# Kernel optimization log

Measured on AMD Instinct MI355X. Metric: run time of the kernel, lower is better.

## Reference

```python
import jax, jax.numpy as jnp
import numpy as np

B, C, H, W = 1, 12, 256, 256
T = 8          # time_steps
F = 64         # recurrent/conv filters
SIGMA = 1.0


def _to_c(x):
    return jax.lax.complex(x[..., 0], x[..., 1])


def _to_r(x):
    return jnp.stack([jnp.real(x), jnp.imag(x)], axis=-1)


def _fft2c(x):  # orthogonal centered 2D FFT over last two dims (complex input)
    x = jnp.fft.ifftshift(x, axes=(-2, -1))
    x = jnp.fft.fft2(x, axes=(-2, -1), norm='ortho')
    return jnp.fft.fftshift(x, axes=(-2, -1))


def _ifft2c(x):
    x = jnp.fft.ifftshift(x, axes=(-2, -1))
    x = jnp.fft.ifft2(x, axes=(-2, -1), norm='ortho')
    return jnp.fft.fftshift(x, axes=(-2, -1))


def _conv(x, w, b=None, dilation=1):
    k = w.shape[-1]
    pad = dilation * (k - 1) // 2  # 'same' padding as ConvNonlinear
    y = jax.lax.conv_general_dilated(x, w, (1, 1), [(pad, pad), (pad, pad)],
                                     rhs_dilation=(dilation, dilation),
                                     dimension_numbers=('NCHW', 'OIHW', 'NCHW'))
    if b is not None:
        y = y + b[None, :, None, None]
    return y


def _gru(x, h, ih_w, ih_b, hh_w, hh_b):  # ConvGRUCell
    i_r, i_z, i_n = jnp.split(_conv(x, ih_w, ih_b), 3, axis=1)
    h_r, h_z, h_n = jnp.split(_conv(h, hh_w, hh_b), 3, axis=1)
    r = jax.nn.sigmoid(i_r + h_r)
    z = jax.nn.sigmoid(i_z + h_z)
    n = jnp.tanh(i_n + r * h_n)
    return (1.0 - z) * n + z * h


def setup_inputs():
    key = jax.random.key(0)
    ks = jax.random.split(key, 16)
    rn = lambda k, s, sc=1.0: jax.random.normal(k, s, jnp.float32) * sc
    return {
        'pred': rn(ks[0], (B, C, H, W, 2)),
        'masked_kspace': rn(ks[1], (B, C, H, W, 2)),
        'sense': rn(ks[2], (B, C, H, W, 2), 0.1),
        'mask': jax.random.randint(ks[3], (B, 1, H, W, 1), 0, 2).astype(bool),
        'conv1_w': rn(ks[4], (F, 4, 5, 5), 0.05),
        'conv1_b': jnp.zeros((F,), jnp.float32),
        'gru1_ih_w': rn(ks[5], (3 * F, F, 1, 1), 0.05),
        'gru1_ih_b': jnp.zeros((3 * F,), jnp.float32),
        'gru1_hh_w': rn(ks[6], (3 * F, F, 1, 1), 0.05),
        'gru1_hh_b': jnp.zeros((3 * F,), jnp.float32),
        'conv2_w': rn(ks[7], (F, F, 3, 3), 0.05),
        'conv2_b': jnp.zeros((F,), jnp.float32),
        'gru2_ih_w': rn(ks[8], (3 * F, F, 1, 1), 0.05),
        'gru2_ih_b': jnp.zeros((3 * F,), jnp.float32),
        'gru2_hh_w': rn(ks[9], (3 * F, F, 1, 1), 0.05),
        'gru2_hh_b': jnp.zeros((3 * F,), jnp.float32),
        'final_w': rn(ks[10], (2, F, 3, 3), 0.05),
        'dc_weight': jnp.ones((1,), jnp.float32),
    }


def reference(pred, masked_kspace, sense, mask, conv1_w, conv1_b, gru1_ih_w, gru1_ih_b,
              gru1_hh_w, gru1_hh_b, conv2_w, conv2_b, gru2_ih_w, gru2_ih_b, gru2_hh_w,
              gru2_hh_b, final_w, dc_weight):
    ksp_c = _to_c(masked_kspace)   # [B,C,H,W] complex
    sense_c = _to_c(sense)
    mask_f = mask[..., 0].astype(jnp.float32)  # [B,1,H,W]
    # eta init (eta=None path): coil-combined ifft of pred
    eta0 = jnp.sum(_ifft2c(_to_c(pred)) * jnp.conj(sense_c), axis=1)  # [B,H,W]
    h1_0 = jnp.zeros((B, F, H, W), jnp.float32)
    h2_0 = jnp.zeros((B, F, H, W), jnp.float32)
    inv_s2 = 1.0 / (SIGMA * SIGMA)

    def step(carry, _):
        eta, h1, h2 = carry
        # log_likelihood_gradient: SENSE-expand, fft, masked residual, ifft, coil-combine
        resid = _ifft2c(mask_f * (_fft2c(eta[:, None] * sense_c) - ksp_c))  # [B,C,H,W]
        grad = jnp.sum(resid * jnp.conj(sense_c), axis=1)                   # [B,H,W]
        g = jnp.stack([eta.real, eta.imag, grad.real, grad.imag], axis=1) * inv_s2  # [B,4,H,W]
        h1 = _gru(jax.nn.relu(_conv(g, conv1_w, conv1_b, 1)), h1,
                  gru1_ih_w, gru1_ih_b, gru1_hh_w, gru1_hh_b)
        h2 = _gru(jax.nn.relu(_conv(h1, conv2_w, conv2_b, 2)), h2,
                  gru2_ih_w, gru2_ih_b, gru2_hh_w, gru2_hh_b)
        d = _conv(h2, final_w, None, 1)  # [B,2,H,W], no bias, no nonlinearity
        eta = eta + jax.lax.complex(d[:, 0], d[:, 1])
        return (eta, h1, h2), eta

    _, etas = jax.lax.scan(step, (eta0, h1_0, h2_0), None, length=T)  # [T,B,H,W]
    # data-consistency output per time step
    soft_dc = jnp.where(mask, pred - masked_kspace, 0.0) * dc_weight[0]  # [B,C,H,W,2]
    dc_c = _to_c(soft_dc)
    out = ksp_c[None] - dc_c[None] - _fft2c(etas[:, :, None] * sense_c[None])  # [T,B,C,H,W]
    return _to_r(out)  # [T,B,C,H,W,2]
```

## Files before the change

kernel.cpp:

```cpp
#include <hip/hip_runtime.h>

#define HW 65536
#define NC 12
#define NF 64
#define NT 8
#define P2 260

typedef float2 c32;
typedef __attribute__((ext_vector_type(8))) short bf16x8;
typedef __attribute__((ext_vector_type(4))) float f32x4;

__device__ __forceinline__ float ssign(int p) {
    return ((p ^ (p >> 8)) & 1) ? -1.0f : 1.0f;
}

__device__ __forceinline__ short f2bf(float f) {
    union { float f; unsigned u; } v; v.f = f;
    unsigned r = (v.u + 0x7FFFu + ((v.u >> 16) & 1u)) >> 16;
    return (short)r;
}

__device__ __forceinline__ float bf2f(unsigned short u) {
    union { unsigned u; float f; } v; v.u = (unsigned)u << 16;
    return v.f;
}

__device__ __forceinline__ void wave_sync() {
    asm volatile("s_waitcnt lgkmcnt(0)" ::: "memory");
}

__device__ __forceinline__ void fft256_wave(c32* X, const c32* tw, int j, float conjf) {
    #pragma unroll
    for (int s = 1; s <= 8; ++s) {
        const int half = 1 << (s - 1);
        #pragma unroll
        for (int b = 0; b < 2; ++b) {
            int idx = j + (b << 6);
            int grp = idx >> (s - 1);
            int pos = idx & (half - 1);
            int i0 = (grp << s) + pos;
            int i1 = i0 + half;
            c32 w = tw[pos << (8 - s)];
            float wy = conjf * w.y;
            c32 a = X[i0], cc = X[i1];
            c32 t = make_float2(w.x * cc.x - wy * cc.y, w.x * cc.y + wy * cc.x);
            X[i0] = make_float2(a.x + t.x, a.y + t.y);
            X[i1] = make_float2(a.x - t.x, a.y - t.y);
        }
        wave_sync();
    }
}

__device__ __forceinline__ void build_tw(c32* tw, int tid) {
    if (tid < 128) {
        float a = -3.14159265358979323846f * (float)tid * (1.0f / 128.0f);
        float sv, cv;
        sincosf(a, &sv, &cv);
        tw[tid] = make_float2(cv, sv);
    }
}

__global__ __launch_bounds__(256) void fft_rows_pre(c32* __restrict__ buf,
        const c32* __restrict__ pred) {
    __shared__ c32 lds[4][256];
    __shared__ c32 tw[128];
    int tid = threadIdx.x;
    build_tw(tw, tid);
    int wid = tid >> 6, j = tid & 63;
    int r = blockIdx.x * 4 + wid;
    int coil = r >> 8, y = r & 255;
    c32* rp = buf + (size_t)r * 256;
    c32* X = lds[wid];
    #pragma unroll
    for (int e = 0; e < 4; ++e) {
        int n = (e << 6) + j;
        float s = ((n + y) & 1) ? -1.0f : 1.0f;
        c32 pv = pred[(size_t)coil * HW + y * 256 + n];
        X[__brev((unsigned)n) >> 24] = make_float2(s * pv.x, s * pv.y);
    }
    __syncthreads();
    fft256_wave(X, tw, j, -1.0f);
    #pragma unroll
    for (int e = 0; e < 4; ++e) {
        int n = (e << 6) + j;
        rp[n] = X[n];
    }
}

__global__ __launch_bounds__(256) void fft_rows_exp(c32* __restrict__ buf,
        const c32* __restrict__ eta, const c32* __restrict__ sense) {
    __shared__ c32 lds[4][256];
    __shared__ c32 tw[128];
    int tid = threadIdx.x;
    build_tw(tw, tid);
    int wid = tid >> 6, j = tid & 63;
    int r = blockIdx.x * 4 + wid;
    int coil = r >> 8, y = r & 255;
    c32* rp = buf + (size_t)r * 256;
    c32* X = lds[wid];
    #pragma unroll
    for (int e = 0; e < 4; ++e) {
        int n = (e << 6) + j;
        float s = ((n + y) & 1) ? -1.0f : 1.0f;
        c32 ev = eta[y * 256 + n];
        c32 sn = sense[(size_t)coil * HW + y * 256 + n];
        X[__brev((unsigned)n) >> 24] =
            make_float2(s * (ev.x * sn.x - ev.y * sn.y),
                        s * (ev.x * sn.y + ev.y * sn.x));
    }
    __syncthreads();
    fft256_wave(X, tw, j, 1.0f);
    #pragma unroll
    for (int e = 0; e < 4; ++e) {
        int n = (e << 6) + j;
        rp[n] = X[n];
    }
}

__global__ __launch_bounds__(256) void fft_rows_grad(const c32* __restrict__ Fk,
        const c32* __restrict__ sense, const c32* __restrict__ eta,
        short* __restrict__ gTp) {
    __shared__ c32 lds[12][256];
    __shared__ c32 tw[128];
    int tid = threadIdx.x;
    build_tw(tw, tid);
    int wid = tid >> 6, j = tid & 63;
    int y = blockIdx.x;
    #pragma unroll
    for (int cc = 0; cc < 3; ++cc) {
        int c = wid * 3 + cc;
        const c32* rp = Fk + (size_t)c * HW + y * 256;
        #pragma unroll
        for (int e = 0; e < 4; ++e) {
            int n = (e << 6) + j;
            lds[c][__brev((unsigned)n) >> 24] = rp[n];
        }
    }
    __syncthreads();
    #pragma unroll
    for (int cc = 0; cc < 3; ++cc)
        fft256_wave(&lds[wid * 3 + cc][0], tw, j, -1.0f);
    __syncthreads();
    int x = tid;
    int p = y * 256 + x;
    float ax = 0.f, ay = 0.f;
    #pragma unroll
    for (int c = 0; c < NC; ++c) {
        c32 t = lds[c][x];
        c32 s = sense[(size_t)c * HW + p];
        ax += t.x * s.x + t.y * s.y;
        ay += t.y * s.x - t.x * s.y;
    }
    float sc = (((x + y) & 1) ? -1.0f : 1.0f) * (1.0f / 256.0f);
    c32 e = eta[p];
    ushort4 o;
    o.x = (unsigned short)f2bf(e.x);
    o.y = (unsigned short)f2bf(e.y);
    o.z = (unsigned short)f2bf(ax * sc);
    o.w = (unsigned short)f2bf(ay * sc);
    ((ushort4*)gTp)[(y + 2) * P2 + x + 2] = o;
}

__global__ __launch_bounds__(256) void fft_cols(c32* __restrict__ buf, float conjf) {
    __shared__ c32 lds[4][257];
    __shared__ c32 tw[128];
    int tid = threadIdx.x;
    build_tw(tw, tid);
    c32* ip = buf + (size_t)blockIdx.y * HW;
    int x0 = blockIdx.x * 4;
    int cl = tid & 3, yb = tid >> 2;
    #pragma unroll
    for (int e = 0; e < 4; ++e) {
        int y = yb + (e << 6);
        lds[cl][__brev((unsigned)y) >> 24] = ip[y * 256 + x0 + cl];
    }
    __syncthreads();
    int col = tid >> 6, j = tid & 63;
    fft256_wave(&lds[col][0], tw, j, conjf);
    __syncthreads();
    #pragma unroll
    for (int e = 0; e < 4; ++e) {
        int y = yb + (e << 6);
        ip[y * 256 + x0 + cl] = lds[cl][y];
    }
}

__global__ __launch_bounds__(256) void fft_cols_fused(c32* __restrict__ buf,
        const c32* __restrict__ base, const c32* __restrict__ ksp,
        const int* __restrict__ mask, c32* __restrict__ outp, int write_out) {
    __shared__ c32 lds[4][257];
    __shared__ c32 tw[128];
    int tid = threadIdx.x;
    build_tw(tw, tid);
    int coil = blockIdx.y;
    c32* ip = buf + (size_t)coil * HW;
    int x0 = blockIdx.x * 4;
    int cl = tid & 3, yb = tid >> 2;
    #pragma unroll
    for (int e = 0; e < 4; ++e) {
        int y = yb + (e << 6);
        lds[cl][__brev((unsigned)y) >> 24] = ip[y * 256 + x0 + cl];
    }
    __syncthreads();
    int col = tid >> 6, j = tid & 63;
    fft256_wave(&lds[col][0], tw, j, 1.0f);
    __syncthreads();

    int x = x0 + cl;
    c32 G[4];
    #pragma unroll
    for (int e = 0; e < 4; ++e) {
        int y = yb + (e << 6);
        G[e] = lds[cl][y];
    }
    __syncthreads();
    #pragma unroll
    for (int e = 0; e < 4; ++e) {
        int y = yb + (e << 6);
        int p = y * 256 + x;
        size_t i = (size_t)coil * HW + p;
        float s = ((p ^ (p >> 8)) & 1) ? -1.0f : 1.0f;
        if (write_out) {
            c32 bv = base[i];
            float sc = s * (1.0f / 256.0f);
            outp[i] = make_float2(bv.x - sc * G[e].x, bv.y - sc * G[e].y);
        }
        c32 rv = make_float2(0.f, 0.f);
        if (mask[p]) {
            c32 k = ksp[i];
            rv = make_float2(G[e].x * (1.0f / 256.0f) - s * k.x,
                             G[e].y * (1.0f / 256.0f) - s * k.y);
        }
        lds[cl][__brev((unsigned)y) >> 24] = rv;
    }
    __syncthreads();
    fft256_wave(&lds[col][0], tw, j, -1.0f);
    __syncthreads();
    #pragma unroll
    for (int e = 0; e < 4; ++e) {
        int y = yb + (e << 6);
        ip[y * 256 + x0 + cl] = lds[cl][y];
    }
}

__global__ __launch_bounds__(256) void k_combine_eta0(const c32* __restrict__ tmp,
        const c32* __restrict__ sense, c32* __restrict__ eta) {
    int p = blockIdx.x * 256 + threadIdx.x;
    float ax = 0.f, ay = 0.f;
    for (int c = 0; c < NC; ++c) {
        c32 t = tmp[c * HW + p], s = sense[c * HW + p];
        ax += t.x * s.x + t.y * s.y;
        ay += t.y * s.x - t.x * s.y;
    }
    float sc = ssign(p) * (1.0f / 256.0f);
    eta[p] = make_float2(ax * sc, ay * sc);
}

__global__ __launch_bounds__(256) void k_base(const c32* __restrict__ ksp,
        const c32* __restrict__ pred, const int* __restrict__ mask,
        const float* __restrict__ dcw, c32* __restrict__ base) {
    int i = blockIdx.x * 256 + threadIdx.x;
    int p = i & (HW - 1);
    c32 k = ksp[i];
    c32 o = k;
    if (mask[p]) {
        float w = dcw[0];
        c32 pr = pred[i];
        o.x -= (pr.x - k.x) * w;
        o.y -= (pr.y - k.y) * w;
    }
    base[i] = o;
}

__global__ __launch_bounds__(256) void k_zero_border(short* __restrict__ gTp,
        short* __restrict__ h1a, short* __restrict__ h1b,
        short* __restrict__ h2a, short* __restrict__ h2b) {
    int i = blockIdx.x * 256 + threadIdx.x;
    if (i >= 2064) return;
    int y, x;
    if (i < 1040) {
        int r = i / 260;
        y = (r < 2) ? r : 256 + r;
        x = i % 260;
    } else {
        int j = i - 1040;
        y = 2 + (j >> 2);
        int cix = j & 3;
        x = (cix < 2) ? cix : 256 + cix;
    }
    size_t px = (size_t)y * P2 + x;
    ((ushort4*)gTp)[px] = make_ushort4(0, 0, 0, 0);
    uint4 z = make_uint4(0, 0, 0, 0);
    uint4* p1 = (uint4*)(h1a + (px << 6));
    uint4* p2 = (uint4*)(h1b + (px << 6));
    uint4* p3 = (uint4*)(h2a + (px << 6));
    uint4* p4 = (uint4*)(h2b + (px << 6));
    #pragma unroll
    for (int e = 0; e < 8; ++e) { p1[e] = z; p2[e] = z; p3[e] = z; p4[e] = z; }
}

__global__ __launch_bounds__(256) void k_prep_c1(const float* __restrict__ w,
        short* __restrict__ wA) {
    int i = blockIdx.x * 256 + threadIdx.x;
    int co = i >> 7, k = i & 127;
    int tap = k >> 2, ci = k & 3;
    float v = (tap < 25) ? w[co * 100 + ci * 25 + tap] : 0.f;
    wA[i] = f2bf(v);
}

__global__ __launch_bounds__(256) void k_prep_c2(const float* __restrict__ w,
        short* __restrict__ wA) {
    int i = blockIdx.x * 256 + threadIdx.x;
    int tap = i >> 12, co = (i >> 6) & 63, ci = i & 63;
    wA[i] = f2bf(w[co * 576 + ci * 9 + tap]);
}

__global__ __launch_bounds__(256) void k_prep_cf(const float* __restrict__ w,
        short* __restrict__ wA) {
    int i = blockIdx.x * 256 + threadIdx.x;
    int tap = i >> 10, r = (i >> 6) & 15, ci = i & 63;
    float v = (r < 2) ? w[r * 576 + ci * 9 + tap] : 0.f;
    wA[i] = f2bf(v);
}

__global__ __launch_bounds__(128) void k_prep_gru(const float* __restrict__ ihw,
        const float* __restrict__ ihb, const float* __restrict__ hhw,
        const float* __restrict__ hhb, short* __restrict__ w2, float* __restrict__ bias) {
    int k = threadIdx.x;
    int r = blockIdx.x;
    int g = r >> 6, co = r & 63;
    float v = 0.f;
    if (g == 0)      v = (k < 64) ? ihw[co * 64 + k]         : hhw[co * 64 + k - 64];
    else if (g == 1) v = (k < 64) ? ihw[(64 + co) * 64 + k]  : hhw[(64 + co) * 64 + k - 64];
    else if (g == 2) v = (k < 64) ? ihw[(128 + co) * 64 + k] : 0.f;
    else             v = (k < 64) ? 0.f : hhw[(128 + co) * 64 + k - 64];
    w2[r * 128 + k] = f2bf(v);
    if (k == 0) {
        float b = (g == 0) ? ihb[co] + hhb[co]
                : (g == 1) ? ihb[64 + co] + hhb[64 + co]
                : (g == 2) ? ihb[128 + co] : hhb[128 + co];
        bias[r] = b;
    }
}

__global__ __launch_bounds__(256, 2) void conv1_mfma(const short* __restrict__ gTp,
        const short* __restrict__ wA, const float* __restrict__ bias,
        short* __restrict__ xT) {
    int wv = threadIdx.x >> 6, l = threadIdx.x & 63;
    int lr = l & 15, lg = l >> 4;
    int y = blockIdx.x >> 3;
    int x0 = (blockIdx.x & 7) << 5;

    bf16x8 A[4];
    const short* pA = wA + (size_t)(wv * 16 + lr) * 128 + lg * 8;
    #pragma unroll
    for (int kt = 0; kt < 4; ++kt) A[kt] = *(const bf16x8*)(pA + kt * 32);

    bf16x8 B[2][4];
    #pragma unroll
    for (int nt = 0; nt < 2; ++nt) {
        int x = x0 + nt * 16 + lr;
        #pragma unroll
        for (int kt = 0; kt < 4; ++kt) {
            int t0 = kt * 8 + lg * 2;
            #pragma unroll
            for (int half = 0; half < 2; ++half) {
                int tap = t0 + half;
                int tt = (tap < 25) ? tap : 0;
                int dy = tt / 5 - 2, dx = tt % 5 - 2;
                ushort4 v = *(const ushort4*)(gTp +
                    ((size_t)((y + dy + 2) * P2 + (x + dx + 2)) << 2));
                B[nt][kt][half * 4 + 0] = (short)v.x;
                B[nt][kt][half * 4 + 1] = (short)v.y;
                B[nt][kt][half * 4 + 2] = (short)v.z;
                B[nt][kt][half * 4 + 3] = (short)v.w;
            }
        }
    }
    f32x4 C[2];
    #pragma unroll
    for (int nt = 0; nt < 2; ++nt) {
        C[nt] = (f32x4){0.f, 0.f, 0.f, 0.f};
        #pragma unroll
        for (int kt = 0; kt < 4; ++kt)
            C[nt] = __builtin_amdgcn_mfma_f32_16x16x32_bf16(A[kt], B[nt][kt], C[nt], 0, 0, 0);
    }
    int co = wv * 16 + lg * 4;
    #pragma unroll
    for (int nt = 0; nt < 2; ++nt) {
        int px = y * 256 + x0 + nt * 16 + lr;
        ushort4 st;
        st.x = (unsigned short)f2bf(fmaxf(C[nt][0] + bias[co + 0], 0.f));
        st.y = (unsigned short)f2bf(fmaxf(C[nt][1] + bias[co + 1], 0.f));
        st.z = (unsigned short)f2bf(fmaxf(C[nt][2] + bias[co + 2], 0.f));
        st.w = (unsigned short)f2bf(fmaxf(C[nt][3] + bias[co + 3], 0.f));
        *(ushort4*)(xT + ((size_t)px << 6) + co) = st;
    }
}

__global__ __launch_bounds__(256, 2) void conv2_mfma(const short* __restrict__ hTp,
        const short* __restrict__ wA, const float* __restrict__ bias,
        short* __restrict__ xT) {
    __shared__ uint4 Ld[3][68][9];
    int tid = threadIdx.x;
    int wv = tid >> 6, l = tid & 63;
    int lr = l & 15, lg = l >> 4;
    int y = blockIdx.x >> 2;
    int x0 = (blockIdx.x & 3) << 6;

    for (int n = tid; n < 3 * 68 * 8; n += 256) {
        int r = n / (68 * 8);
        int rem = n - r * (68 * 8);
        int px = rem >> 3, e = rem & 7;
        const uint4* src = (const uint4*)(hTp +
            (((size_t)(y + 2 * r) * P2 + (x0 + px)) << 6)) + e;
        Ld[r][px][e] = *src;
    }
    __syncthreads();

    f32x4 C[4];
    #pragma unroll
    for (int nt = 0; nt < 4; ++nt) C[nt] = (f32x4){0.f, 0.f, 0.f, 0.f};

    #pragma unroll
    for (int tap = 0; tap < 9; ++tap) {
        int r = tap / 3;
        int dx = (tap % 3 - 1) * 2;
        const short* pA = wA + (size_t)(tap * 64 + wv * 16 + lr) * 64 + lg * 8;
        bf16x8 A0 = *(const bf16x8*)(pA);
        bf16x8 A1 = *(const bf16x8*)(pA + 32);
        #pragma unroll
        for (int nt = 0; nt < 4; ++nt) {
            int xl = nt * 16 + lr + dx + 2;
            bf16x8 B0 = *(const bf16x8*)&Ld[r][xl][lg];
            bf16x8 B1 = *(const bf16x8*)&Ld[r][xl][4 + lg];
            C[nt] = __builtin_amdgcn_mfma_f32_16x16x32_bf16(A0, B0, C[nt], 0, 0, 0);
            C[nt] = __builtin_amdgcn_mfma_f32_16x16x32_bf16(A1, B1, C[nt], 0, 0, 0);
        }
    }
    int co = wv * 16 + lg * 4;
    #pragma unroll
    for (int nt = 0; nt < 4; ++nt) {
        int px = y * 256 + x0 + nt * 16 + lr;
        ushort4 st;
        st.x = (unsigned short)f2bf(fmaxf(C[nt][0] + bias[co + 0], 0.f));
        st.y = (unsigned short)f2bf(fmaxf(C[nt][1] + bias[co + 1], 0.f));
        st.z = (unsigned short)f2bf(fmaxf(C[nt][2] + bias[co + 2], 0.f));
        st.w = (unsigned short)f2bf(fmaxf(C[nt][3] + bias[co + 3], 0.f));
        *(ushort4*)(xT + ((size_t)px << 6) + co) = st;
    }
}

template <bool FIRST>
__global__ __launch_bounds__(256, 2) void gru_mfma(const short* __restrict__ xT,
        const short* __restrict__ hprev, const short* __restrict__ w2,
        const float* __restrict__ bias, short* __restrict__ hnext) {
    int wv = threadIdx.x >> 6, l = threadIdx.x & 63;
    int lr = l & 15, lg = l >> 4;
    int px0 = blockIdx.x * 64;

    bf16x8 A0[4], A1[4], A2[2], A3[2];
    {
        const short* w0 = w2 + (0   + wv * 16 + lr) * 128 + lg * 8;
        const short* w1 = w2 + (64  + wv * 16 + lr) * 128 + lg * 8;
        const short* w2p = w2 + (128 + wv * 16 + lr) * 128 + lg * 8;
        const short* w3 = w2 + (192 + wv * 16 + lr) * 128 + lg * 8;
        #pragma unroll
        for (int kt = 0; kt < 4; ++kt) {
            A0[kt] = *(const bf16x8*)(w0 + kt * 32);
            A1[kt] = *(const bf16x8*)(w1 + kt * 32);
        }
        A2[0] = *(const bf16x8*)(w2p);          A2[1] = *(const bf16x8*)(w2p + 32);
        A3[0] = *(const bf16x8*)(w3 + 64);      A3[1] = *(const bf16x8*)(w3 + 96);
    }

    f32x4 C0[4], C1[4], C2[4], C3[4];
    #pragma unroll
    for (int nt = 0; nt < 4; ++nt) {
        C0[nt] = (f32x4){0.f, 0.f, 0.f, 0.f};
        C1[nt] = (f32x4){0.f, 0.f, 0.f, 0.f};
        C2[nt] = (f32x4){0.f, 0.f, 0.f, 0.f};
        C3[nt] = (f32x4){0.f, 0.f, 0.f, 0.f};
    }

    #pragma unroll
    for (int nt = 0; nt < 4; ++nt) {
        int px = px0 + nt * 16 + lr;
        int yy = px >> 8, xx = px & 255;
        size_t pb = ((size_t)((yy + 2) * P2 + (xx + 2)) << 6);
        bf16x8 B0 = *(const bf16x8*)(xT + ((size_t)px << 6) + lg * 8);
        bf16x8 B1 = *(const bf16x8*)(xT + ((size_t)px << 6) + 32 + lg * 8);
        C0[nt] = __builtin_amdgcn_mfma_f32_16x16x32_bf16(A0[0], B0, C0[nt], 0, 0, 0);
        C0[nt] = __builtin_amdgcn_mfma_f32_16x16x32_bf16(A0[1], B1, C0[nt], 0, 0, 0);
        C1[nt] = __builtin_amdgcn_mfma_f32_16x16x32_bf16(A1[0], B0, C1[nt], 0, 0, 0);
        C1[nt] = __builtin_amdgcn_mfma_f32_16x16x32_bf16(A1[1], B1, C1[nt], 0, 0, 0);
        C2[nt] = __builtin_amdgcn_mfma_f32_16x16x32_bf16(A2[0], B0, C2[nt], 0, 0, 0);
        C2[nt] = __builtin_amdgcn_mfma_f32_16x16x32_bf16(A2[1], B1, C2[nt], 0, 0, 0);
        if (!FIRST) {
            bf16x8 B2 = *(const bf16x8*)(hprev + pb + lg * 8);
            bf16x8 B3 = *(const bf16x8*)(hprev + pb + 32 + lg * 8);
            C0[nt] = __builtin_amdgcn_mfma_f32_16x16x32_bf16(A0[2], B2, C0[nt], 0, 0, 0);
            C0[nt] = __builtin_amdgcn_mfma_f32_16x16x32_bf16(A0[3], B3, C0[nt], 0, 0, 0);
            C1[nt] = __builtin_amdgcn_mfma_f32_16x16x32_bf16(A1[2], B2, C1[nt], 0, 0, 0);
            C1[nt] = __builtin_amdgcn_mfma_f32_16x16x32_bf16(A1[3], B3, C1[nt], 0, 0, 0);
            C3[nt] = __builtin_amdgcn_mfma_f32_16x16x32_bf16(A3[0], B2, C3[nt], 0, 0, 0);
            C3[nt] = __builtin_amdgcn_mfma_f32_16x16x32_bf16(A3[1], B3, C3[nt], 0, 0, 0);
        }
    }

    int co = wv * 16 + lg * 4;
    float br[4], bz[4], bin_[4], bhn[4];
    #pragma unroll
    for (int i = 0; i < 4; ++i) {
        br[i]   = bias[co + i];
        bz[i]   = bias[64 + co + i];
        bin_[i] = bias[128 + co + i];
        bhn[i]  = bias[192 + co + i];
    }
    #pragma unroll
    for (int nt = 0; nt < 4; ++nt) {
        int px = px0 + nt * 16 + lr;
        int yy = px >> 8, xx = px & 255;
        size_t pb = ((size_t)((yy + 2) * P2 + (xx + 2)) << 6);
        ushort4 hov = make_ushort4(0, 0, 0, 0);
        if (!FIRST) hov = *(const ushort4*)(hprev + pb + co);
        float ho[4] = {bf2f(hov.x), bf2f(hov.y), bf2f(hov.z), bf2f(hov.w)};
        ushort4 st;
        unsigned short* sp = &st.x;
        #pragma unroll
        for (int i = 0; i < 4; ++i) {
            float r = 1.0f / (1.0f + expf(-(C0[nt][i] + br[i])));
            float z = 1.0f / (1.0f + expf(-(C1[nt][i] + bz[i])));
            float nn = tanhf(C2[nt][i] + bin_[i] + r * (C3[nt][i] + bhn[i]));
            float hv = FIRST ? (1.0f - z) * nn : (1.0f - z) * nn + z * ho[i];
            sp[i] = (unsigned short)f2bf(hv);
        }
        *(ushort4*)(hnext + pb + co) = st;
    }
}

__global__ __launch_bounds__(256, 2) void final_mfma(const short* __restrict__ hTp,
        const short* __restrict__ wA, c32* __restrict__ eta) {
    int wv = threadIdx.x >> 6, l = threadIdx.x & 63;
    int lr = l & 15, lg = l >> 4;
    int y = blockIdx.x >> 2;
    int x0 = (blockIdx.x & 3) << 6;
    int x = x0 + wv * 16 + lr;

    auto loadB = [&](int tap, bf16x8& b0, bf16x8& b1) {
        int dy = tap / 3 - 1, dx = tap % 3 - 1;
        const short* pB = hTp +
            ((size_t)((y + dy + 2) * P2 + (x + dx + 2)) << 6) + lg * 8;
        b0 = *(const bf16x8*)(pB);
        b1 = *(const bf16x8*)(pB + 32);
    };

    f32x4 C = (f32x4){0.f, 0.f, 0.f, 0.f};
    bf16x8 cB0, cB1;
    loadB(0, cB0, cB1);
    #pragma unroll
    for (int tap = 0; tap < 9; ++tap) {
        const short* pA = wA + (size_t)(tap * 16 + lr) * 64 + lg * 8;
        bf16x8 A0 = *(const bf16x8*)(pA);
        bf16x8 A1 = *(const bf16x8*)(pA + 32);
        bf16x8 nB0, nB1;
        if (tap < 8) loadB(tap + 1, nB0, nB1);
        C = __builtin_amdgcn_mfma_f32_16x16x32_bf16(A0, cB0, C, 0, 0, 0);
        C = __builtin_amdgcn_mfma_f32_16x16x32_bf16(A1, cB1, C, 0, 0, 0);
        if (tap < 8) { cB0 = nB0; cB1 = nB1; }
    }
    if (lg == 0) {
        int px = y * 256 + x;
        c32 e = eta[px];
        eta[px] = make_float2(e.x + C[0], e.y + C[1]);
    }
}

extern "C" void kernel_launch(void* const* d_in, const int* in_sizes, int n_in,
                              void* d_out, int out_size, void* d_ws, size_t ws_size,
                              hipStream_t stream) {
    const c32* pred   = (const c32*)d_in[0];
    const c32* ksp    = (const c32*)d_in[1];
    const c32* sense  = (const c32*)d_in[2];
    const int* mask   = (const int*)d_in[3];
    const float* c1w  = (const float*)d_in[4];
    const float* c1b  = (const float*)d_in[5];
    const float* g1iw = (const float*)d_in[6];
    const float* g1ib = (const float*)d_in[7];
    const float* g1hw = (const float*)d_in[8];
    const float* g1hb = (const float*)d_in[9];
    const float* c2w  = (const float*)d_in[10];
    const float* c2b  = (const float*)d_in[11];
    const float* g2iw = (const float*)d_in[12];
    const float* g2ib = (const float*)d_in[13];
    const float* g2hw = (const float*)d_in[14];
    const float* g2hb = (const float*)d_in[15];
    const float* fw   = (const float*)d_in[16];
    const float* dcw  = (const float*)d_in[17];

    const size_t PP = (size_t)P2 * P2;
    float* w0 = (float*)d_ws;
    c32* base = (c32*)w0;
    c32* Fk   = base + NC * HW;
    c32* tmp  = Fk + NC * HW;
    c32* eta  = tmp + NC * HW;
    short* gTp = (short*)(eta + HW);
    short* xT  = gTp + PP * 4;
    short* h1Ta = xT + (size_t)HW * 64;
    short* h1Tb = h1Ta + PP * 64;
    short* h2Ta = h1Tb + PP * 64;
    short* h2Tb = h2Ta + PP * 64;
    short* w2a  = h2Tb + PP * 64;
    short* w2b  = w2a + 256 * 128;
    float* biasA = (float*)(w2b + 256 * 128);
    float* biasB = biasA + 256;
    short* wAc2 = (short*)(biasB + 256);
    short* wAc1 = wAc2 + 9 * 64 * 64;
    short* wAcf = wAc1 + 64 * 128;

    dim3 B(256);
    const int gCHW = NC * HW / 256;
    const int gHW  = HW / 256;
    const int gROW = NC * 256 / 4;
    dim3 gCOL(64, NC);
    const int gGRU = HW / 64;
    const int gCNV = HW / 32;

    k_zero_border<<<9, B, 0, stream>>>(gTp, h1Ta, h1Tb, h2Ta, h2Tb);
    k_prep_gru<<<256, 128, 0, stream>>>(g1iw, g1ib, g1hw, g1hb, w2a, biasA);
    k_prep_gru<<<256, 128, 0, stream>>>(g2iw, g2ib, g2hw, g2hb, w2b, biasB);
    k_prep_c2<<<144, 256, 0, stream>>>(c2w, wAc2);
    k_prep_c1<<<32, 256, 0, stream>>>(c1w, wAc1);
    k_prep_cf<<<36, 256, 0, stream>>>(fw, wAcf);

    fft_rows_pre<<<gROW, B, 0, stream>>>(tmp, pred);
    fft_cols<<<gCOL, B, 0, stream>>>(tmp, -1.0f);
    k_combine_eta0<<<gHW, B, 0, stream>>>(tmp, sense, eta);

    k_base<<<gCHW, B, 0, stream>>>(ksp, pred, mask, dcw, base);

    fft_rows_exp<<<gROW, B, 0, stream>>>(Fk, eta, sense);
    fft_cols_fused<<<gCOL, B, 0, stream>>>(Fk, base, ksp, mask, (c32*)d_out, 0);

    short* h1c = h1Ta; short* h1n = h1Tb;
    short* h2c = h2Ta; short* h2n = h2Tb;
    c32* outp = (c32*)d_out;

    for (int t = 0; t < NT; ++t) {
        fft_rows_grad<<<gHW, B, 0, stream>>>(Fk, sense, eta, gTp);

        conv1_mfma<<<gCNV, B, 0, stream>>>(gTp, wAc1, c1b, xT);
        if (t == 0) {
            gru_mfma<true><<<gGRU, B, 0, stream>>>(xT, h1c, w2a, biasA, h1n);
        } else {
            gru_mfma<false><<<gGRU, B, 0, stream>>>(xT, h1c, w2a, biasA, h1n);
        }
        { short* s = h1c; h1c = h1n; h1n = s; }
        conv2_mfma<<<gGRU, B, 0, stream>>>(h1c, wAc2, c2b, xT);
        if (t == 0) {
            gru_mfma<true><<<gGRU, B, 0, stream>>>(xT, h2c, w2b, biasB, h2n);
        } else {
            gru_mfma<false><<<gGRU, B, 0, stream>>>(xT, h2c, w2b, biasB, h2n);
        }
        { short* s = h2c; h2c = h2n; h2n = s; }
        final_mfma<<<gGRU, B, 0, stream>>>(h2c, wAcf, eta);

        fft_rows_exp<<<gROW, B, 0, stream>>>(Fk, eta, sense);
        fft_cols_fused<<<gCOL, B, 0, stream>>>(Fk, base, ksp, mask,
                                               outp + (size_t)t * NC * HW, 1);
    }
}
```

Baseline: 978.5 us.

## Fuse conv1/conv2 with following ConvGRU cells via shared-memory handoff

Merges each convolution kernel with its subsequent GRU kernel. The relu-activated conv output is staged in an LDS tile (padded rows of 68) and consumed directly by a shared gru_tail routine, which removes the xT global round trip and two launches per time step. The price is extra LDS per block, higher register pressure in the fused kernels, and for conv1 the GRU now runs on 32-pixel tiles, so each block reloads the GRU weights for half as many pixels.

Result: faster. 918.2 us (-6.2%).

```diff
diff --git a/kernel.cpp b/kernel.cpp
--- a/kernel.cpp
+++ b/kernel.cpp
@@ -343,9 +343,98 @@
     }
 }
 
-__global__ __launch_bounds__(256, 2) void conv1_mfma(const short* __restrict__ gTp,
-        const short* __restrict__ wA, const float* __restrict__ bias,
-        short* __restrict__ xT) {
+template <int NTN, bool FIRST>
+__device__ __forceinline__ void gru_tail(const short (*xch)[68],
+        const short* __restrict__ hprev, const short* __restrict__ w2,
+        const float* __restrict__ bias, short* __restrict__ hnext,
+        int wv, int lr, int lg, int px0 ) {
+    bf16x8 A0[4], A1[4], A2[2], A3[2];
+    {
+        const short* w0 = w2 + (0   + wv * 16 + lr) * 128 + lg * 8;
+        const short* w1 = w2 + (64  + wv * 16 + lr) * 128 + lg * 8;
+        const short* w2p = w2 + (128 + wv * 16 + lr) * 128 + lg * 8;
+        const short* w3 = w2 + (192 + wv * 16 + lr) * 128 + lg * 8;
+        #pragma unroll
+        for (int kt = 0; kt < 4; ++kt) {
+            A0[kt] = *(const bf16x8*)(w0 + kt * 32);
+            A1[kt] = *(const bf16x8*)(w1 + kt * 32);
+        }
+        A2[0] = *(const bf16x8*)(w2p);          A2[1] = *(const bf16x8*)(w2p + 32);
+        A3[0] = *(const bf16x8*)(w3 + 64);      A3[1] = *(const bf16x8*)(w3 + 96);
+    }
+
+    f32x4 C0[NTN], C1[NTN], C2[NTN], C3[NTN];
+    #pragma unroll
+    for (int nt = 0; nt < NTN; ++nt) {
+        C0[nt] = (f32x4){0.f, 0.f, 0.f, 0.f};
+        C1[nt] = (f32x4){0.f, 0.f, 0.f, 0.f};
+        C2[nt] = (f32x4){0.f, 0.f, 0.f, 0.f};
+        C3[nt] = (f32x4){0.f, 0.f, 0.f, 0.f};
+    }
+
+    #pragma unroll
+    for (int nt = 0; nt < NTN; ++nt) {
+        int pxl = nt * 16 + lr;
+        int px = px0 + pxl;
+        int yy = px >> 8, xx = px & 255;
+        size_t pb = ((size_t)((yy + 2) * P2 + (xx + 2)) << 6);
+        bf16x8 B0 = *(const bf16x8*)&xch[pxl][lg * 8];
+        bf16x8 B1 = *(const bf16x8*)&xch[pxl][32 + lg * 8];
+        C0[nt] = __builtin_amdgcn_mfma_f32_16x16x32_bf16(A0[0], B0, C0[nt], 0, 0, 0);
+        C0[nt] = __builtin_amdgcn_mfma_f32_16x16x32_bf16(A0[1], B1, C0[nt], 0, 0, 0);
+        C1[nt] = __builtin_amdgcn_mfma_f32_16x16x32_bf16(A1[0], B0, C1[nt], 0, 0, 0);
+        C1[nt] = __builtin_amdgcn_mfma_f32_16x16x32_bf16(A1[1], B1, C1[nt], 0, 0, 0);
+        C2[nt] = __builtin_amdgcn_mfma_f32_16x16x32_bf16(A2[0], B0, C2[nt], 0, 0, 0);
+        C2[nt] = __builtin_amdgcn_mfma_f32_16x16x32_bf16(A2[1], B1, C2[nt], 0, 0, 0);
+        if (!FIRST) {
+            bf16x8 B2 = *(const bf16x8*)(hprev + pb + lg * 8);
+            bf16x8 B3 = *(const bf16x8*)(hprev + pb + 32 + lg * 8);
+            C0[nt] = __builtin_amdgcn_mfma_f32_16x16x32_bf16(A0[2], B2, C0[nt], 0, 0, 0);
+            C0[nt] = __builtin_amdgcn_mfma_f32_16x16x32_bf16(A0[3], B3, C0[nt], 0, 0, 0);
+            C1[nt] = __builtin_amdgcn_mfma_f32_16x16x32_bf16(A1[2], B2, C1[nt], 0, 0, 0);
+            C1[nt] = __builtin_amdgcn_mfma_f32_16x16x32_bf16(A1[3], B3, C1[nt], 0, 0, 0);
+            C3[nt] = __builtin_amdgcn_mfma_f32_16x16x32_bf16(A3[0], B2, C3[nt], 0, 0, 0);
+            C3[nt] = __builtin_amdgcn_mfma_f32_16x16x32_bf16(A3[1], B3, C3[nt], 0, 0, 0);
+        }
+    }
+
+    int co = wv * 16 + lg * 4;
+    float br[4], bz[4], bin_[4], bhn[4];
+    #pragma unroll
+    for (int i = 0; i < 4; ++i) {
+        br[i]   = bias[co + i];
+        bz[i]   = bias[64 + co + i];
+        bin_[i] = bias[128 + co + i];
+        bhn[i]  = bias[192 + co + i];
+    }
+    #pragma unroll
+    for (int nt = 0; nt < NTN; ++nt) {
+        int px = px0 + nt * 16 + lr;
+        int yy = px >> 8, xx = px & 255;
+        size_t pb = ((size_t)((yy + 2) * P2 + (xx + 2)) << 6);
+        ushort4 hov = make_ushort4(0, 0, 0, 0);
+        if (!FIRST) hov = *(const ushort4*)(hprev + pb + co);
+        float ho[4] = {bf2f(hov.x), bf2f(hov.y), bf2f(hov.z), bf2f(hov.w)};
+        ushort4 st;
+        unsigned short* sp = &st.x;
+        #pragma unroll
+        for (int i = 0; i < 4; ++i) {
+            float r = 1.0f / (1.0f + expf(-(C0[nt][i] + br[i])));
+            float z = 1.0f / (1.0f + expf(-(C1[nt][i] + bz[i])));
+            float nn = tanhf(C2[nt][i] + bin_[i] + r * (C3[nt][i] + bhn[i]));
+            float hv = FIRST ? (1.0f - z) * nn : (1.0f - z) * nn + z * ho[i];
+            sp[i] = (unsigned short)f2bf(hv);
+        }
+        *(ushort4*)(hnext + pb + co) = st;
+    }
+}
+
+template <bool FIRST>
+__global__ __launch_bounds__(256, 2) void conv1_gru1(const short* __restrict__ gTp,
+        const short* __restrict__ wA, const float* __restrict__ cbias,
+        const short* __restrict__ w2, const float* __restrict__ gbias,
+        const short* __restrict__ hprev, short* __restrict__ hnext) {
+    __shared__ short xch[32][68];
     int wv = threadIdx.x >> 6, l = threadIdx.x & 63;
     int lr = l & 15, lg = l >> 4;
     int y = blockIdx.x >> 3;
@@ -377,31 +466,32 @@
             }
         }
     }
-    f32x4 C[2];
+    int co = wv * 16 + lg * 4;
     #pragma unroll
     for (int nt = 0; nt < 2; ++nt) {
-        C[nt] = (f32x4){0.f, 0.f, 0.f, 0.f};
+        f32x4 C = (f32x4){0.f, 0.f, 0.f, 0.f};
         #pragma unroll
         for (int kt = 0; kt < 4; ++kt)
-            C[nt] = __builtin_amdgcn_mfma_f32_16x16x32_bf16(A[kt], B[nt][kt], C[nt], 0, 0, 0);
-    }
-    int co = wv * 16 + lg * 4;
-    #pragma unroll
-    for (int nt = 0; nt < 2; ++nt) {
-        int px = y * 256 + x0 + nt * 16 + lr;
+            C = __builtin_amdgcn_mfma_f32_16x16x32_bf16(A[kt], B[nt][kt], C, 0, 0, 0);
         ushort4 st;
-        st.x = (unsigned short)f2bf(fmaxf(C[nt][0] + bias[co + 0], 0.f));
-        st.y = (unsigned short)f2bf(fmaxf(C[nt][1] + bias[co + 1], 0.f));
-        st.z = (unsigned short)f2bf(fmaxf(C[nt][2] + bias[co + 2], 0.f));
-        st.w = (unsigned short)f2bf(fmaxf(C[nt][3] + bias[co + 3], 0.f));
-        *(ushort4*)(xT + ((size_t)px << 6) + co) = st;
-    }
-}
-
-__global__ __launch_bounds__(256, 2) void conv2_mfma(const short* __restrict__ hTp,
-        const short* __restrict__ wA, const float* __restrict__ bias,
-        short* __restrict__ xT) {
+        st.x = (unsigned short)f2bf(fmaxf(C[0] + cbias[co + 0], 0.f));
+        st.y = (unsigned short)f2bf(fmaxf(C[1] + cbias[co + 1], 0.f));
+        st.z = (unsigned short)f2bf(fmaxf(C[2] + cbias[co + 2], 0.f));
+        st.w = (unsigned short)f2bf(fmaxf(C[3] + cbias[co + 3], 0.f));
+        *(ushort4*)&xch[nt * 16 + lr][co] = st;
+    }
+    __syncthreads();
+
+    gru_tail<2, FIRST>(xch, hprev, w2, gbias, hnext, wv, lr, lg, y * 256 + x0);
+}
+
+template <bool FIRST>
+__global__ __launch_bounds__(256, 2) void conv2_gru2(const short* __restrict__ h1Tp,
+        const short* __restrict__ wA, const float* __restrict__ cbias,
+        const short* __restrict__ w2, const float* __restrict__ gbias,
+        const short* __restrict__ hprev, short* __restrict__ hnext) {
     __shared__ uint4 Ld[3][68][9];
+    __shared__ short xch[64][68];
     int tid = threadIdx.x;
     int wv = tid >> 6, l = tid & 63;
     int lr = l & 15, lg = l >> 4;
@@ -412,7 +502,7 @@
         int r = n / (68 * 8);
         int rem = n - r * (68 * 8);
         int px = rem >> 3, e = rem & 7;
-        const uint4* src = (const uint4*)(hTp +
+        const uint4* src = (const uint4*)(h1Tp +
             (((size_t)(y + 2 * r) * P2 + (x0 + px)) << 6)) + e;
         Ld[r][px][e] = *src;
     }
@@ -441,102 +531,16 @@
     int co = wv * 16 + lg * 4;
     #pragma unroll
     for (int nt = 0; nt < 4; ++nt) {
-        int px = y * 256 + x0 + nt * 16 + lr;
         ushort4 st;
-        st.x = (unsigned short)f2bf(fmaxf(C[nt][0] + bias[co + 0], 0.f));
-        st.y = (unsigned short)f2bf(fmaxf(C[nt][1] + bias[co + 1], 0.f));
-        st.z = (unsigned short)f2bf(fmaxf(C[nt][2] + bias[co + 2], 0.f));
-        st.w = (unsigned short)f2bf(fmaxf(C[nt][3] + bias[co + 3], 0.f));
-        *(ushort4*)(xT + ((size_t)px << 6) + co) = st;
-    }
-}
-
-template <bool FIRST>
-__global__ __launch_bounds__(256, 2) void gru_mfma(const short* __restrict__ xT,
-        const short* __restrict__ hprev, const short* __restrict__ w2,
-        const float* __restrict__ bias, short* __restrict__ hnext) {
-    int wv = threadIdx.x >> 6, l = threadIdx.x & 63;
-    int lr = l & 15, lg = l >> 4;
-    int px0 = blockIdx.x * 64;
-
-    bf16x8 A0[4], A1[4], A2[2], A3[2];
-    {
-        const short* w0 = w2 + (0   + wv * 16 + lr) * 128 + lg * 8;
-        const short* w1 = w2 + (64  + wv * 16 + lr) * 128 + lg * 8;
-        const short* w2p = w2 + (128 + wv * 16 + lr) * 128 + lg * 8;
-        const short* w3 = w2 + (192 + wv * 16 + lr) * 128 + lg * 8;
-        #pragma unroll
-        for (int kt = 0; kt < 4; ++kt) {
-            A0[kt] = *(const bf16x8*)(w0 + kt * 32);
-            A1[kt] = *(const bf16x8*)(w1 + kt * 32);
-        }
-        A2[0] = *(const bf16x8*)(w2p);          A2[1] = *(const bf16x8*)(w2p + 32);
-        A3[0] = *(const bf16x8*)(w3 + 64);      A3[1] = *(const bf16x8*)(w3 + 96);
-    }
-
-    f32x4 C0[4], C1[4], C2[4], C3[4];
-    #pragma unroll
-    for (int nt = 0; nt < 4; ++nt) {
-        C0[nt] = (f32x4){0.f, 0.f, 0.f, 0.f};
-        C1[nt] = (f32x4){0.f, 0.f, 0.f, 0.f};
-        C2[nt] = (f32x4){0.f, 0.f, 0.f, 0.f};
-        C3[nt] = (f32x4){0.f, 0.f, 0.f, 0.f};
-    }
-
-    #pragma unroll
-    for (int nt = 0; nt < 4; ++nt) {
-        int px = px0 + nt * 16 + lr;
-        int yy = px >> 8, xx = px & 255;
-        size_t pb = ((size_t)((yy + 2) * P2 + (xx + 2)) << 6);
-        bf16x8 B0 = *(const bf16x8*)(xT + ((size_t)px << 6) + lg * 8);
-        bf16x8 B1 = *(const bf16x8*)(xT + ((size_t)px << 6) + 32 + lg * 8);
-        C0[nt] = __builtin_amdgcn_mfma_f32_16x16x32_bf16(A0[0], B0, C0[nt], 0, 0, 0);
-        C0[nt] = __builtin_amdgcn_mfma_f32_16x16x32_bf16(A0[1], B1, C0[nt], 0, 0, 0);
-        C1[nt] = __builtin_amdgcn_mfma_f32_16x16x32_bf16(A1[0], B0, C1[nt], 0, 0, 0);
-        C1[nt] = __builtin_amdgcn_mfma_f32_16x16x32_bf16(A1[1], B1, C1[nt], 0, 0, 0);
-        C2[nt] = __builtin_amdgcn_mfma_f32_16x16x32_bf16(A2[0], B0, C2[nt], 0, 0, 0);
-        C2[nt] = __builtin_amdgcn_mfma_f32_16x16x32_bf16(A2[1], B1, C2[nt], 0, 0, 0);
-        if (!FIRST) {
-            bf16x8 B2 = *(const bf16x8*)(hprev + pb + lg * 8);
-            bf16x8 B3 = *(const bf16x8*)(hprev + pb + 32 + lg * 8);
-            C0[nt] = __builtin_amdgcn_mfma_f32_16x16x32_bf16(A0[2], B2, C0[nt], 0, 0, 0);
-            C0[nt] = __builtin_amdgcn_mfma_f32_16x16x32_bf16(A0[3], B3, C0[nt], 0, 0, 0);
-            C1[nt] = __builtin_amdgcn_mfma_f32_16x16x32_bf16(A1[2], B2, C1[nt], 0, 0, 0);
-            C1[nt] = __builtin_amdgcn_mfma_f32_16x16x32_bf16(A1[3], B3, C1[nt], 0, 0, 0);
-            C3[nt] = __builtin_amdgcn_mfma_f32_16x16x32_bf16(A3[0], B2, C3[nt], 0, 0, 0);
-            C3[nt] = __builtin_amdgcn_mfma_f32_16x16x32_bf16(A3[1], B3, C3[nt], 0, 0, 0);
-        }
-    }
-
-    int co = wv * 16 + lg * 4;
-    float br[4], bz[4], bin_[4], bhn[4];
-    #pragma unroll
-    for (int i = 0; i < 4; ++i) {
-        br[i]   = bias[co + i];
-        bz[i]   = bias[64 + co + i];
-        bin_[i] = bias[128 + co + i];
-        bhn[i]  = bias[192 + co + i];
-    }
-    #pragma unroll
-    for (int nt = 0; nt < 4; ++nt) {
-        int px = px0 + nt * 16 + lr;
-        int yy = px >> 8, xx = px & 255;
-        size_t pb = ((size_t)((yy + 2) * P2 + (xx + 2)) << 6);
-        ushort4 hov = make_ushort4(0, 0, 0, 0);
-        if (!FIRST) hov = *(const ushort4*)(hprev + pb + co);
-        float ho[4] = {bf2f(hov.x), bf2f(hov.y), bf2f(hov.z), bf2f(hov.w)};
-        ushort4 st;
-        unsigned short* sp = &st.x;
-        #pragma unroll
-        for (int i = 0; i < 4; ++i) {
-            float r = 1.0f / (1.0f + expf(-(C0[nt][i] + br[i])));
-            float z = 1.0f / (1.0f + expf(-(C1[nt][i] + bz[i])));
-            float nn = tanhf(C2[nt][i] + bin_[i] + r * (C3[nt][i] + bhn[i]));
-            float hv = FIRST ? (1.0f - z) * nn : (1.0f - z) * nn + z * ho[i];
-            sp[i] = (unsigned short)f2bf(hv);
-        }
-        *(ushort4*)(hnext + pb + co) = st;
-    }
+        st.x = (unsigned short)f2bf(fmaxf(C[nt][0] + cbias[co + 0], 0.f));
+        st.y = (unsigned short)f2bf(fmaxf(C[nt][1] + cbias[co + 1], 0.f));
+        st.z = (unsigned short)f2bf(fmaxf(C[nt][2] + cbias[co + 2], 0.f));
+        st.w = (unsigned short)f2bf(fmaxf(C[nt][3] + cbias[co + 3], 0.f));
+        *(ushort4*)&xch[nt * 16 + lr][co] = st;
+    }
+    __syncthreads();
+
+    gru_tail<4, FIRST>(xch, hprev, w2, gbias, hnext, wv, lr, lg, y * 256 + x0);
 }
 
 __global__ __launch_bounds__(256, 2) void final_mfma(const short* __restrict__ hTp,
@@ -605,8 +609,7 @@
     c32* tmp  = Fk + NC * HW;
     c32* eta  = tmp + NC * HW;
     short* gTp = (short*)(eta + HW);
-    short* xT  = gTp + PP * 4;
-    short* h1Ta = xT + (size_t)HW * 64;
+    short* h1Ta = gTp + PP * 4;
     short* h1Tb = h1Ta + PP * 64;
     short* h2Ta = h1Tb + PP * 64;
     short* h2Tb = h2Ta + PP * 64;
@@ -623,8 +626,8 @@
     const int gHW  = HW / 256;
     const int gROW = NC * 256 / 4;
     dim3 gCOL(64, NC);
-    const int gGRU = HW / 64;
-    const int gCNV = HW / 32;
+    const int gC1 = HW / 32;
+    const int gC2 = HW / 64;
 
     k_zero_border<<<9, B, 0, stream>>>(gTp, h1Ta, h1Tb, h2Ta, h2Tb);
     k_prep_gru<<<256, 128, 0, stream>>>(g1iw, g1ib, g1hw, g1hb, w2a, biasA);
@@ -649,21 +652,19 @@
     for (int t = 0; t < NT; ++t) {
         fft_rows_grad<<<gHW, B, 0, stream>>>(Fk, sense, eta, gTp);
 
-        conv1_mfma<<<gCNV, B, 0, stream>>>(gTp, wAc1, c1b, xT);
         if (t == 0) {
-            gru_mfma<true><<<gGRU, B, 0, stream>>>(xT, h1c, w2a, biasA, h1n);
+            conv1_gru1<true><<<gC1, B, 0, stream>>>(gTp, wAc1, c1b, w2a, biasA, h1c, h1n);
         } else {
-            gru_mfma<false><<<gGRU, B, 0, stream>>>(xT, h1c, w2a, biasA, h1n);
+            conv1_gru1<false><<<gC1, B, 0, stream>>>(gTp, wAc1, c1b, w2a, biasA, h1c, h1n);
         }
         { short* s = h1c; h1c = h1n; h1n = s; }
-        conv2_mfma<<<gGRU, B, 0, stream>>>(h1c, wAc2, c2b, xT);
         if (t == 0) {
-            gru_mfma<true><<<gGRU, B, 0, stream>>>(xT, h2c, w2b, biasB, h2n);
+            conv2_gru2<true><<<gC2, B, 0, stream>>>(h1c, wAc2, c2b, w2b, biasB, h2c, h2n);
         } else {
-            gru_mfma<false><<<gGRU, B, 0, stream>>>(xT, h2c, w2b, biasB, h2n);
+            conv2_gru2<false><<<gC2, B, 0, stream>>>(h1c, wAc2, c2b, w2b, biasB, h2c, h2n);
         }
         { short* s = h2c; h2c = h2n; h2n = s; }
-        final_mfma<<<gGRU, B, 0, stream>>>(h2c, wAcf, eta);
+        final_mfma<<<gC2, B, 0, stream>>>(h2c, wAcf, eta);
 
         fft_rows_exp<<<gROW, B, 0, stream>>>(Fk, eta, sense);
         fft_cols_fused<<<gCOL, B, 0, stream>>>(Fk, base, ksp, mask,
```
